# Kernel optimization log

Measured on AMD Instinct MI355X. Metric: run time of the kernel, lower is better.

The kernel has to match this reference:

```python
import jax, jax.numpy as jnp
import numpy as np

B, L, E, H = 4, 1024, 2048, 16
DH = E // H
SCALE_BASE = 512.0


def _rotate_every_two(x):
    x1 = x[..., ::2]
    x2 = x[..., 1::2]
    return jnp.stack([-x2, x1], axis=-1).reshape(x.shape)


def _xpos(x, downscale):
    # x: [BH, L, Dh]; non-incremental path => offset = 0
    length = x.shape[1]
    head_dim = x.shape[-1]
    min_pos = -(length // 2)
    positions = jnp.arange(min_pos, length + min_pos, dtype=jnp.float32)  # [L]
    base = (jnp.arange(0, head_dim, 2, dtype=jnp.float32) + 0.4 * head_dim) / (1.4 * head_dim)  # [Dh/2]
    scale = base[None, :] ** (positions[:, None] / SCALE_BASE)  # [L, Dh/2]
    # fixed_pos_embedding over `scale` (seq_len=L, dim=Dh/2), positions 0..L-1
    dim = head_dim // 2
    inv_freq = 1.0 / (10000.0 ** (jnp.arange(0, dim, dtype=jnp.float32) / dim))
    sinusoid = jnp.arange(length, dtype=jnp.float32)[:, None] * inv_freq[None, :]
    sin, cos = jnp.sin(sinusoid), jnp.cos(sinusoid)
    if downscale:
        scale = 1.0 / scale
    sin_s = jnp.repeat(sin * scale, 2, axis=-1)  # duplicate_interleave -> [L, Dh]
    cos_s = jnp.repeat(cos * scale, 2, axis=-1)
    return x * cos_s + _rotate_every_two(x) * sin_s


def setup_inputs() -> dict:
    key = jax.random.key(0)
    ks = jax.random.split(key, 6)
    w_std = 1.0 / np.sqrt(E)
    query = jax.random.normal(ks[0], (B, L, E), dtype=jnp.float32)
    Wq = jax.random.normal(ks[1], (E, E), dtype=jnp.float32) * w_std
    Wk = jax.random.normal(ks[2], (E, E), dtype=jnp.float32) * w_std
    Wv = jax.random.normal(ks[3], (E, E), dtype=jnp.float32) * w_std
    Wo = jax.random.normal(ks[4], (E, E), dtype=jnp.float32) * w_std
    bq = jnp.zeros((E,), jnp.float32)
    bk = jnp.zeros((E,), jnp.float32)
    bv = jnp.zeros((E,), jnp.float32)
    bo = jnp.zeros((E,), jnp.float32)
    # causal additive mask [L, L]: 0 on/below diag, large negative above
    attn_mask = jnp.where(jnp.triu(jnp.ones((L, L), bool), k=1), -1e9, 0.0).astype(jnp.float32)
    rel_pos = jax.random.normal(ks[5], (B * H, L, L), dtype=jnp.float32) * 0.02
    return {"query": query, "Wq": Wq, "bq": bq, "Wk": Wk, "bk": bk, "Wv": Wv,
            "bv": bv, "Wo": Wo, "bo": bo, "attn_mask": attn_mask, "rel_pos": rel_pos}


def reference(query, Wq, bq, Wk, bk, Wv, bv, Wo, bo, attn_mask, rel_pos):
    scaling = DH ** -0.5
    q = (query @ Wq.T + bq) * scaling
    k = query @ Wk.T + bk
    v = query @ Wv.T + bv

    def split(t):  # [B, L, E] -> [B*H, L, Dh]
        return t.reshape(B, L, H, DH).transpose(0, 2, 1, 3).reshape(B * H, L, DH)

    q, k, v = split(q), split(k), split(v)
    k = _xpos(k, downscale=True)
    q = _xpos(q, downscale=False)

    w = jnp.einsum('btd,bsd->bts', q, k)          # [B*H, L, L]
    w = jnp.nan_to_num(w) + attn_mask[None]
    w = w + rel_pos
    w = jax.nn.softmax(w.astype(jnp.float32), axis=-1).astype(w.dtype)
    attn = jnp.einsum('bts,bsd->btd', w, v)       # [B*H, L, Dh]
    attn = attn.reshape(B, H, L, DH).transpose(0, 2, 1, 3).reshape(B, L, E)
    out = attn @ Wo.T + bo
    attn_weights = w.reshape(B, H, L, L).transpose(1, 0, 2, 3)  # [H, B, L, L]
    return out, attn_weights
```

## Files before the change

### kernel.cpp

```cpp
#include <hip/hip_runtime.h>
#include <math.h>

#define BB 4
#define LL 1024
#define EE 2048
#define HH 16
#define DHD 128
#define NTOK 4096
#define NBH 64
#define OUT0_ELEMS 8388608

typedef __attribute__((ext_vector_type(8))) short short8;
typedef __attribute__((ext_vector_type(4))) float f32x4;
typedef __attribute__((ext_vector_type(4))) unsigned short ushort4v;
typedef __attribute__((ext_vector_type(8))) unsigned short ushort8v;

__device__ __forceinline__ unsigned short f2bf(float x) {
    union { float f; unsigned int u; } v; v.f = x;
    unsigned int r = v.u + 0x7FFFu + ((v.u >> 16) & 1u);
    return (unsigned short)(r >> 16);
}
__device__ __forceinline__ float bf2f(unsigned short h) {
    union { unsigned int u; float f; } v; v.u = ((unsigned int)h) << 16;
    return v.f;
}

__device__ __forceinline__ void gload16(const void* g, void* l) {
    __builtin_amdgcn_global_load_lds((const __attribute__((address_space(1))) void*)g,
                                     (__attribute__((address_space(3))) void*)l,
                                     16, 0, 0);
}

__global__ __launch_bounds__(256) void cvt_k(const float* __restrict__ in,
                                             unsigned short* __restrict__ out, int n) {
    int i = (blockIdx.x * 256 + threadIdx.x) * 8;
    if (i >= n) return;
    float4 a = *(const float4*)(in + i);
    float4 b = *(const float4*)(in + i + 4);
    ushort4v u, w;
    u.x = f2bf(a.x); u.y = f2bf(a.y); u.z = f2bf(a.z); u.w = f2bf(a.w);
    w.x = f2bf(b.x); w.y = f2bf(b.y); w.z = f2bf(b.z); w.w = f2bf(b.w);
    *(ushort4v*)(out + i) = u;
    *(ushort4v*)(out + i + 4) = w;
}

__global__ __launch_bounds__(64) void xpos_table_k(float4* __restrict__ tab) {
    int t = blockIdx.x;
    int j = threadIdx.x;
    float pos = (float)(t - 512);
    float base = (2.0f * (float)j + 51.2f) * (1.0f / 179.2f);
    float sc = powf(base, pos * (1.0f / 512.0f));
    float inv_freq = powf(10000.0f, -(float)j * (1.0f / 64.0f));
    float ang = (float)t * inv_freq;
    float s = sinf(ang);
    float c = cosf(ang);
    tab[(t << 6) | j] = make_float4(c * sc, s * sc, c / sc, s / sc);
}

__global__ __launch_bounds__(256) void xpos_apply_k(unsigned short* __restrict__ q,
                                                    unsigned short* __restrict__ k,
                                                    const float4* __restrict__ tab) {
    int g = blockIdx.x * 256 + threadIdx.x;
    int jj = g & 15;
    int t = (g >> 4) & 1023;
    int bh = g >> 14;
    size_t off = (((size_t)((bh << 10) | t)) << 7) + jj * 8;
    ushort8v qv = *(const ushort8v*)(q + off);
    ushort8v kv = *(const ushort8v*)(k + off);
    ushort8v qo, ko;
#pragma unroll
    for (int p = 0; p < 4; ++p) {
        float4 tb = tab[(t << 6) | (jj * 4 + p)];
        float qx = bf2f(qv[2 * p]), qy = bf2f(qv[2 * p + 1]);
        float kx = bf2f(kv[2 * p]), ky = bf2f(kv[2 * p + 1]);
        qo[2 * p]     = f2bf(qx * tb.x - qy * tb.y);
        qo[2 * p + 1] = f2bf(qy * tb.x + qx * tb.y);
        ko[2 * p]     = f2bf(kx * tb.z - ky * tb.w);
        ko[2 * p + 1] = f2bf(ky * tb.z + kx * tb.w);
    }
    *(ushort8v*)(q + off) = qo;
    *(ushort8v*)(k + off) = ko;
}

template <int MODE>
__global__ __launch_bounds__(256)
void mm_k(const unsigned short* __restrict__ Abf, const unsigned short* __restrict__ Bp,
          const float* __restrict__ bias, void* __restrict__ Cptr, float alpha) {
    __shared__ alignas(16) unsigned short lA[128 * 32];
    __shared__ alignas(16) unsigned short lB[128 * 32];

    const int tid = threadIdx.x;
    const int lane = tid & 63;
    const int wave = tid >> 6;
    const int wr = wave >> 1, wc = wave & 1;
    const int fr = lane & 15, fq = lane >> 4;
    const int m0 = blockIdx.y * 128, n0 = blockIdx.x * 128;

    f32x4 acc[4][4];
#pragma unroll
    for (int i = 0; i < 4; ++i)
#pragma unroll
        for (int j = 0; j < 4; ++j) acc[i][j] = (f32x4){0.f, 0.f, 0.f, 0.f};

    for (int k0 = 0; k0 < 2048; k0 += 32) {
#pragma unroll
        for (int i = 0; i < 2; ++i) {
            int c = i * 256 + tid;
            int r = c >> 2, kc = c & 3;
            gload16(Abf + (size_t)(m0 + r) * 2048 + k0 + kc * 8, &lA[c * 8]);
        }
#pragma unroll
        for (int i = 0; i < 2; ++i) {
            int c = i * 256 + tid;
            int r = c >> 2, kc = c & 3;
            gload16(Bp + (size_t)(n0 + r) * 2048 + k0 + kc * 8, &lB[c * 8]);
        }
        __syncthreads();

        short8 afr[4], bfr[4];
#pragma unroll
        for (int mi = 0; mi < 4; ++mi)
            afr[mi] = *(const short8*)&lA[(wr * 64 + mi * 16 + fr) * 32 + fq * 8];
#pragma unroll
        for (int ni = 0; ni < 4; ++ni)
            bfr[ni] = *(const short8*)&lB[(wc * 64 + ni * 16 + fr) * 32 + fq * 8];
#pragma unroll
        for (int mi = 0; mi < 4; ++mi)
#pragma unroll
            for (int ni = 0; ni < 4; ++ni)
                acc[mi][ni] = __builtin_amdgcn_mfma_f32_16x16x32_bf16(
                    afr[mi], bfr[ni], acc[mi][ni], 0, 0, 0);
        __syncthreads();
    }

#pragma unroll
    for (int mi = 0; mi < 4; ++mi) {
#pragma unroll
        for (int ni = 0; ni < 4; ++ni) {
#pragma unroll
            for (int r = 0; r < 4; ++r) {
                int m = m0 + wr * 64 + mi * 16 + fq * 4 + r;
                int n = n0 + wc * 64 + ni * 16 + fr;
                float v = acc[mi][ni][r];
                if constexpr (MODE == 0 || MODE == 1) {
                    v = alpha * (v + bias[n]);
                    int b_ = m >> 10, t = m & 1023, h = n >> 7, d = n & 127;
                    unsigned short* q = (unsigned short*)Cptr;
                    q[(((size_t)(b_ * HH + h) << 10 | t) << 7) | d] = f2bf(v);
                } else if constexpr (MODE == 2) {
                    v += bias[n];
                    int b_ = m >> 10, t = m & 1023, h = n >> 7, d = n & 127;
                    unsigned short* vt = (unsigned short*)Cptr;
                    vt[((size_t)(b_ * HH + h) * 128 + d) * 1024 + t] = f2bf(v);
                } else {
                    float* C = (float*)Cptr;
                    C[(size_t)m * EE + n] = v + bias[n];
                }
            }
        }
    }
}

__global__ __launch_bounds__(256)
void scores_k(const unsigned short* __restrict__ qb, const unsigned short* __restrict__ kb,
              const float* __restrict__ rel, float* __restrict__ attnP,
              float* __restrict__ psum) {
    __shared__ alignas(16) char smem[16384];
    unsigned short* lA = (unsigned short*)smem;
    unsigned short* lB = (unsigned short*)(smem + 8192);
    float* slab = (float*)smem;

    const int tid = threadIdx.x;
    const int lane = tid & 63, wave = tid >> 6;
    const int wr = wave >> 1, wc = wave & 1;
    const int fr = lane & 15, fq = lane >> 4;

    int idx = blockIdx.x;
    int tt = (int)((sqrtf(8.f * (float)idx + 1.f) - 1.f) * 0.5f);
    while ((tt + 1) * (tt + 2) / 2 <= idx) ++tt;
    while (tt * (tt + 1) / 2 > idx) --tt;
    const int ss = idx - tt * (tt + 1) / 2;
    const int t0 = tt << 7, s0 = ss << 7;
    const int bh = blockIdx.y;
    const int hh = bh & 15, bb = bh >> 4;

    const unsigned short* Q = qb + ((size_t)bh << 17);
    const unsigned short* K = kb + ((size_t)bh << 17);

    f32x4 acc[4][4];
#pragma unroll
    for (int i = 0; i < 4; ++i)
#pragma unroll
        for (int j = 0; j < 4; ++j) acc[i][j] = (f32x4){0.f, 0.f, 0.f, 0.f};

    for (int k0 = 0; k0 < 128; k0 += 32) {
#pragma unroll
        for (int i = 0; i < 2; ++i) {
            int c = i * 256 + tid;
            int r = c >> 2, kc = c & 3;
            gload16(Q + (size_t)(t0 + r) * 128 + k0 + kc * 8, &lA[c * 8]);
        }
#pragma unroll
        for (int i = 0; i < 2; ++i) {
            int c = i * 256 + tid;
            int r = c >> 2, kc = c & 3;
            gload16(K + (size_t)(s0 + r) * 128 + k0 + kc * 8, &lB[c * 8]);
        }
        __syncthreads();

        short8 afr[4], bfr[4];
#pragma unroll
        for (int mi = 0; mi < 4; ++mi)
            afr[mi] = *(const short8*)&lA[(wr * 64 + mi * 16 + fr) * 32 + fq * 8];
#pragma unroll
        for (int ni = 0; ni < 4; ++ni)
            bfr[ni] = *(const short8*)&lB[(wc * 64 + ni * 16 + fr) * 32 + fq * 8];
#pragma unroll
        for (int mi = 0; mi < 4; ++mi)
#pragma unroll
            for (int ni = 0; ni < 4; ++ni)
                acc[mi][ni] = __builtin_amdgcn_mfma_f32_16x16x32_bf16(
                    afr[mi], bfr[ni], acc[mi][ni], 0, 0, 0);
        __syncthreads();
    }

    float* PO = attnP + (((size_t)(hh * BB + bb)) << 20);
    const float* RLb = rel + ((size_t)bh << 20);
#pragma unroll
    for (int sl = 0; sl < 4; ++sl) {
        if (wr == (sl >> 1)) {
#pragma unroll
            for (int mi2 = 0; mi2 < 2; ++mi2) {
                int mi = ((sl & 1) << 1) + mi2;
#pragma unroll
                for (int ni = 0; ni < 4; ++ni)
#pragma unroll
                    for (int r = 0; r < 4; ++r) {
                        int srow = (mi2 << 4) + (fq << 2) + r;
                        int col = (wc << 6) + (ni << 4) + fr;
                        slab[srow * 128 + (col ^ (((srow >> 2) & 3) << 4))] = acc[mi][ni][r];
                    }
            }
        }
        __syncthreads();
        {
            int srow = tid >> 3;
            int tg = t0 + (sl << 5) + srow;
            const float* RL = RLb + ((size_t)tg << 10) + s0;
            float* PR = PO + ((size_t)tg << 10) + s0;
            float rsum = 0.f;
#pragma unroll
            for (int c = 0; c < 4; ++c) {
                int col = ((tid & 7) << 2) + (c << 5);
                float4 sv = *(const float4*)&slab[srow * 128 + (col ^ (((srow >> 2) & 3) << 4))];
                float4 rl = *(const float4*)(RL + col);
                float4 e;
                e.x = (s0 + col     <= tg) ? __expf(sv.x + rl.x - 15.f) : 0.f;
                e.y = (s0 + col + 1 <= tg) ? __expf(sv.y + rl.y - 15.f) : 0.f;
                e.z = (s0 + col + 2 <= tg) ? __expf(sv.z + rl.z - 15.f) : 0.f;
                e.w = (s0 + col + 3 <= tg) ? __expf(sv.w + rl.w - 15.f) : 0.f;
                *(float4*)(PR + col) = e;
                rsum += e.x + e.y + e.z + e.w;
            }
            rsum += __shfl_xor(rsum, 1);
            rsum += __shfl_xor(rsum, 2);
            rsum += __shfl_xor(rsum, 4);
            if ((tid & 7) == 0)
                psum[((((size_t)bh << 10) + tg) << 3) + ss] = rsum;
        }
        __syncthreads();
    }
}

__global__ __launch_bounds__(256)
void pv_k(const float* __restrict__ attnP, const unsigned short* __restrict__ vt,
          const float* __restrict__ psum, unsigned short* __restrict__ am) {
    __shared__ alignas(16) unsigned short lA[128 * 32];
    __shared__ alignas(16) unsigned short lB[128 * 32];
    __shared__ float lInv[128];

    const int tid = threadIdx.x;
    const int lane = tid & 63, wave = tid >> 6;
    const int wr = wave >> 1, wc = wave & 1;
    const int fr = lane & 15, fq = lane >> 4;
    const int tt = 7 - blockIdx.x;
    const int t0 = tt << 7;
    const int bh = blockIdx.y;
    const int hh = bh & 15, bb = bh >> 4;

    const float* PO = attnP + (((size_t)(hh * BB + bb)) << 20) + ((size_t)t0 << 10);
    const unsigned short* Vb = vt + ((size_t)bh << 17);

    if (tid < 128) {
        const float* p = psum + ((((size_t)bh << 10) + t0 + tid) << 3);
        float s = 0.f;
#pragma unroll
        for (int j = 0; j < 8; ++j) s += (j <= tt) ? p[j] : 0.f;
        lInv[tid] = 1.f / s;
    }

    f32x4 acc[4][4];
#pragma unroll
    for (int i = 0; i < 4; ++i)
#pragma unroll
        for (int j = 0; j < 4; ++j) acc[i][j] = (f32x4){0.f, 0.f, 0.f, 0.f};

    const int kend = (tt + 1) << 7;
    for (int k0 = 0; k0 < kend; k0 += 32) {
#pragma unroll
        for (int i = 0; i < 4; ++i) {
            int c = i * 256 + tid;
            int r = c >> 3, cc = c & 7;
            float4 v = *(const float4*)(PO + (size_t)r * 1024 + k0 + cc * 4);
            ushort4v h;
            h.x = f2bf(v.x); h.y = f2bf(v.y); h.z = f2bf(v.z); h.w = f2bf(v.w);
            *(ushort4v*)&lA[r * 32 + cc * 4] = h;
        }
#pragma unroll
        for (int i = 0; i < 2; ++i) {
            int c = i * 256 + tid;
            int r = c >> 2, kc = c & 3;
            gload16(Vb + (size_t)r * 1024 + k0 + kc * 8, &lB[c * 8]);
        }
        __syncthreads();

        short8 afr[4], bfr[4];
#pragma unroll
        for (int mi = 0; mi < 4; ++mi)
            afr[mi] = *(const short8*)&lA[(wr * 64 + mi * 16 + fr) * 32 + fq * 8];
#pragma unroll
        for (int ni = 0; ni < 4; ++ni)
            bfr[ni] = *(const short8*)&lB[(wc * 64 + ni * 16 + fr) * 32 + fq * 8];
#pragma unroll
        for (int mi = 0; mi < 4; ++mi)
#pragma unroll
            for (int ni = 0; ni < 4; ++ni)
                acc[mi][ni] = __builtin_amdgcn_mfma_f32_16x16x32_bf16(
                    afr[mi], bfr[ni], acc[mi][ni], 0, 0, 0);
        __syncthreads();
    }

#pragma unroll
    for (int mi = 0; mi < 4; ++mi)
#pragma unroll
        for (int ni = 0; ni < 4; ++ni)
#pragma unroll
            for (int r = 0; r < 4; ++r) {
                int tl = wr * 64 + mi * 16 + fq * 4 + r;
                int d = wc * 64 + ni * 16 + fr;
                float o = acc[mi][ni][r] * lInv[tl];
                am[(((size_t)(bb * 1024 + t0 + tl)) << 11) + hh * 128 + d] = f2bf(o);
            }
}

__global__ __launch_bounds__(256)
void norm_k(float* __restrict__ attnP, const float* __restrict__ psum) {
    const int tid = threadIdx.x;
    const int lane = tid & 63, wave = tid >> 6;
    const int row = blockIdx.x * 4 + wave;
    const int bh = row >> 10, t = row & 1023;
    const int hh = bh & 15, bb = bh >> 4;
    const int tt = t >> 7;
    float v = (lane < 8 && lane <= tt) ? psum[((size_t)row << 3) + lane] : 0.f;
    v += __shfl_xor(v, 1);
    v += __shfl_xor(v, 2);
    v += __shfl_xor(v, 4);
    float inv = 1.f / __shfl(v, 0);
    float* PR = attnP + (((size_t)(hh * BB + bb)) << 20) + ((size_t)t << 10);
#pragma unroll
    for (int it = 0; it < 4; ++it) {
        int col = it * 256 + lane * 4;
        if (col <= t) {
            float4 x = *(const float4*)(PR + col);
            x.x *= inv; x.y *= inv; x.z *= inv; x.w *= inv;
            *(float4*)(PR + col) = x;
        } else {
            *(float4*)(PR + col) = make_float4(0.f, 0.f, 0.f, 0.f);
        }
    }
}

extern "C" void kernel_launch(void* const* d_in, const int* in_sizes, int n_in,
                              void* d_out, int out_size, void* d_ws, size_t ws_size,
                              hipStream_t stream) {
    const float* query = (const float*)d_in[0];
    const float* Wq    = (const float*)d_in[1];
    const float* bq    = (const float*)d_in[2];
    const float* Wk    = (const float*)d_in[3];
    const float* bk    = (const float*)d_in[4];
    const float* Wv    = (const float*)d_in[5];
    const float* bv    = (const float*)d_in[6];
    const float* Wo    = (const float*)d_in[7];
    const float* bo    = (const float*)d_in[8];
    const float* rel   = (const float*)d_in[10];

    float* out    = (float*)d_out;
    float* attn_w = out + OUT0_ELEMS;

    char* w = (char*)d_ws;
    unsigned short* Xbf = (unsigned short*)(w);
    unsigned short* Wqb = (unsigned short*)(w + (16 << 20));
    unsigned short* Wkb = (unsigned short*)(w + (24 << 20));
    unsigned short* Wvb = (unsigned short*)(w + (32 << 20));
    unsigned short* Wob = (unsigned short*)(w + (40 << 20));
    unsigned short* qb  = (unsigned short*)(w + (48 << 20));
    unsigned short* kb  = (unsigned short*)(w + (64 << 20));
    unsigned short* vt  = (unsigned short*)(w + (80 << 20));
    unsigned short* am  = (unsigned short*)(w + (96 << 20));
    float4* tab         = (float4*)(w + (112 << 20));
    float* psum         = (float*)(w + (113u << 20));

    const float scaling = 0.08838834764831845f;

    xpos_table_k<<<LL, 64, 0, stream>>>(tab);

    cvt_k<<<4096, 256, 0, stream>>>(query, Xbf, OUT0_ELEMS);
    cvt_k<<<2048, 256, 0, stream>>>(Wq, Wqb, EE * EE);
    cvt_k<<<2048, 256, 0, stream>>>(Wk, Wkb, EE * EE);
    cvt_k<<<2048, 256, 0, stream>>>(Wv, Wvb, EE * EE);
    cvt_k<<<2048, 256, 0, stream>>>(Wo, Wob, EE * EE);

    dim3 gproj(EE / 128, NTOK / 128, 1);
    mm_k<0><<<gproj, 256, 0, stream>>>(Xbf, Wqb, bq, qb, scaling);
    mm_k<1><<<gproj, 256, 0, stream>>>(Xbf, Wkb, bk, kb, 1.0f);
    mm_k<2><<<gproj, 256, 0, stream>>>(Xbf, Wvb, bv, vt, 1.0f);

    xpos_apply_k<<<(NBH * LL * 16) / 256, 256, 0, stream>>>(qb, kb, tab);

    dim3 gsc(36, NBH);
    scores_k<<<gsc, 256, 0, stream>>>(qb, kb, rel, attn_w, psum);

    dim3 gpv(8, NBH);
    pv_k<<<gpv, 256, 0, stream>>>(attn_w, vt, psum, am);

    norm_k<<<NBH * LL / 4, 256, 0, stream>>>(attn_w, psum);

    dim3 gout(EE / 128, NTOK / 128, 1);
    mm_k<4><<<gout, 256, 0, stream>>>(am, Wob, bo, out, 1.0f);
}
```

Baseline: 498.8 us.

## Fuse QKV projections into one GEMM and fold softmax normalization into PV

Packs Wq/Wk/Wv contiguously and launches a single QKV projection GEMM over a 3x wider grid, selecting bias, scale and output layout per block. Removes the separate norm kernel by having pv_k scale each probability row by its inverse sum while loading it, write the normalized values back to the attention-weights output, and zero the masked tail region. This avoids one extra full read/write pass over the large fp32 attention tensor and two kernel launches, at the cost of pv_k now doing read-modify-write stores and extra zero-fill stores. Also moves the normalization before the bf16 conversion, changing rounding slightly.

```diff
diff --git a/kernel.cpp b/kernel.cpp
--- a/kernel.cpp
+++ b/kernel.cpp
@@ -82,10 +82,12 @@
     *(ushort8v*)(k + off) = ko;
 }
 
-template <int MODE>
 __global__ __launch_bounds__(256)
-void mm_k(const unsigned short* __restrict__ Abf, const unsigned short* __restrict__ Bp,
-          const float* __restrict__ bias, void* __restrict__ Cptr, float alpha) {
+void mmqkv_k(const unsigned short* __restrict__ Abf, const unsigned short* __restrict__ Wqkv,
+             const float* __restrict__ bq, const float* __restrict__ bk,
+             const float* __restrict__ bv, unsigned short* __restrict__ qb,
+             unsigned short* __restrict__ kb, unsigned short* __restrict__ vt,
+             float scaling) {
     __shared__ alignas(16) unsigned short lA[128 * 32];
     __shared__ alignas(16) unsigned short lB[128 * 32];
 
@@ -95,6 +97,9 @@
     const int wr = wave >> 1, wc = wave & 1;
     const int fr = lane & 15, fq = lane >> 4;
     const int m0 = blockIdx.y * 128, n0 = blockIdx.x * 128;
+    const int w = n0 >> 11;
+    const float* bsel = (w == 0) ? bq : (w == 1) ? bk : bv;
+    const float alpha = (w == 0) ? scaling : 1.0f;
 
     f32x4 acc[4][4];
 #pragma unroll
@@ -113,7 +118,7 @@
         for (int i = 0; i < 2; ++i) {
             int c = i * 256 + tid;
             int r = c >> 2, kc = c & 3;
-            gload16(Bp + (size_t)(n0 + r) * 2048 + k0 + kc * 8, &lB[c * 8]);
+            gload16(Wqkv + (size_t)(n0 + r) * 2048 + k0 + kc * 8, &lB[c * 8]);
         }
         __syncthreads();
 
@@ -141,24 +146,80 @@
             for (int r = 0; r < 4; ++r) {
                 int m = m0 + wr * 64 + mi * 16 + fq * 4 + r;
                 int n = n0 + wc * 64 + ni * 16 + fr;
-                float v = acc[mi][ni][r];
-                if constexpr (MODE == 0 || MODE == 1) {
-                    v = alpha * (v + bias[n]);
-                    int b_ = m >> 10, t = m & 1023, h = n >> 7, d = n & 127;
-                    unsigned short* q = (unsigned short*)Cptr;
-                    q[(((size_t)(b_ * HH + h) << 10 | t) << 7) | d] = f2bf(v);
-                } else if constexpr (MODE == 2) {
-                    v += bias[n];
-                    int b_ = m >> 10, t = m & 1023, h = n >> 7, d = n & 127;
-                    unsigned short* vt = (unsigned short*)Cptr;
-                    vt[((size_t)(b_ * HH + h) * 128 + d) * 1024 + t] = f2bf(v);
-                } else {
-                    float* C = (float*)Cptr;
-                    C[(size_t)m * EE + n] = v + bias[n];
-                }
+                int nn = n & 2047;
+                int b_ = m >> 10, t = m & 1023, h = nn >> 7, d = nn & 127;
+                float v = alpha * (acc[mi][ni][r] + bsel[nn]);
+                if (w == 0)
+                    qb[(((size_t)(b_ * HH + h) << 10 | t) << 7) | d] = f2bf(v);
+                else if (w == 1)
+                    kb[(((size_t)(b_ * HH + h) << 10 | t) << 7) | d] = f2bf(v);
+                else
+                    vt[((size_t)((b_ * HH + h) * 128 + d) << 10) | t] = f2bf(v);
             }
         }
     }
+}
+
+__global__ __launch_bounds__(256)
+void mmo_k(const unsigned short* __restrict__ Abf, const unsigned short* __restrict__ Bp,
+           const float* __restrict__ bias, float* __restrict__ C) {
+    __shared__ alignas(16) unsigned short lA[128 * 32];
+    __shared__ alignas(16) unsigned short lB[128 * 32];
+
+    const int tid = threadIdx.x;
+    const int lane = tid & 63;
+    const int wave = tid >> 6;
+    const int wr = wave >> 1, wc = wave & 1;
+    const int fr = lane & 15, fq = lane >> 4;
+    const int m0 = blockIdx.y * 128, n0 = blockIdx.x * 128;
+
+    f32x4 acc[4][4];
+#pragma unroll
+    for (int i = 0; i < 4; ++i)
+#pragma unroll
+        for (int j = 0; j < 4; ++j) acc[i][j] = (f32x4){0.f, 0.f, 0.f, 0.f};
+
+    for (int k0 = 0; k0 < 2048; k0 += 32) {
+#pragma unroll
+        for (int i = 0; i < 2; ++i) {
+            int c = i * 256 + tid;
+            int r = c >> 2, kc = c & 3;
+            gload16(Abf + (size_t)(m0 + r) * 2048 + k0 + kc * 8, &lA[c * 8]);
+        }
+#pragma unroll
+        for (int i = 0; i < 2; ++i) {
+            int c = i * 256 + tid;
+            int r = c >> 2, kc = c & 3;
+            gload16(Bp + (size_t)(n0 + r) * 2048 + k0 + kc * 8, &lB[c * 8]);
+        }
+        __syncthreads();
+
+        short8 afr[4], bfr[4];
+#pragma unroll
+        for (int mi = 0; mi < 4; ++mi)
+            afr[mi] = *(const short8*)&lA[(wr * 64 + mi * 16 + fr) * 32 + fq * 8];
+#pragma unroll
+        for (int ni = 0; ni < 4; ++ni)
+            bfr[ni] = *(const short8*)&lB[(wc * 64 + ni * 16 + fr) * 32 + fq * 8];
+#pragma unroll
+        for (int mi = 0; mi < 4; ++mi)
+#pragma unroll
+            for (int ni = 0; ni < 4; ++ni)
+                acc[mi][ni] = __builtin_amdgcn_mfma_f32_16x16x32_bf16(
+                    afr[mi], bfr[ni], acc[mi][ni], 0, 0, 0);
+        __syncthreads();
+    }
+
+#pragma unroll
+    for (int mi = 0; mi < 4; ++mi)
+#pragma unroll
+        for (int ni = 0; ni < 4; ++ni)
+#pragma unroll
+            for (int r = 0; r < 4; ++r) {
+                int m = m0 + wr * 64 + mi * 16 + fq * 4 + r;
+                int n = n0 + wc * 64 + ni * 16 + fr;
+                C[(size_t)m * EE + n] = acc[mi][ni][r] + bias[n];
+            }
 }
 
 __global__ __launch_bounds__(256)
@@ -273,7 +334,7 @@
 }
 
 __global__ __launch_bounds__(256)
-void pv_k(const float* __restrict__ attnP, const unsigned short* __restrict__ vt,
+void pv_k(float* __restrict__ attnP, const unsigned short* __restrict__ vt,
           const float* __restrict__ psum, unsigned short* __restrict__ am) {
     __shared__ alignas(16) unsigned short lA[128 * 32];
     __shared__ alignas(16) unsigned short lB[128 * 32];
@@ -288,7 +349,7 @@
     const int bh = blockIdx.y;
     const int hh = bh & 15, bb = bh >> 4;
 
-    const float* PO = attnP + (((size_t)(hh * BB + bb)) << 20) + ((size_t)t0 << 10);
+    float* PO = attnP + (((size_t)(hh * BB + bb)) << 20) + ((size_t)t0 << 10);
     const unsigned short* Vb = vt + ((size_t)bh << 17);
 
     if (tid < 128) {
@@ -298,6 +359,7 @@
         for (int j = 0; j < 8; ++j) s += (j <= tt) ? p[j] : 0.f;
         lInv[tid] = 1.f / s;
     }
+    __syncthreads();
 
     f32x4 acc[4][4];
 #pragma unroll
@@ -311,7 +373,11 @@
         for (int i = 0; i < 4; ++i) {
             int c = i * 256 + tid;
             int r = c >> 3, cc = c & 7;
-            float4 v = *(const float4*)(PO + (size_t)r * 1024 + k0 + cc * 4);
+            float* gp = PO + (size_t)r * 1024 + k0 + cc * 4;
+            float4 v = *(const float4*)gp;
+            float inv = lInv[r];
+            v.x *= inv; v.y *= inv; v.z *= inv; v.w *= inv;
+            *(float4*)gp = v;
             ushort4v h;
             h.x = f2bf(v.x); h.y = f2bf(v.y); h.z = f2bf(v.z); h.w = f2bf(v.w);
             *(ushort4v*)&lA[r * 32 + cc * 4] = h;
@@ -348,35 +414,15 @@
             for (int r = 0; r < 4; ++r) {
                 int tl = wr * 64 + mi * 16 + fq * 4 + r;
                 int d = wc * 64 + ni * 16 + fr;
-                float o = acc[mi][ni][r] * lInv[tl];
-                am[(((size_t)(bb * 1024 + t0 + tl)) << 11) + hh * 128 + d] = f2bf(o);
+                am[(((size_t)(bb * 1024 + t0 + tl)) << 11) + hh * 128 + d] =
+                    f2bf(acc[mi][ni][r]);
             }
-}
-
-__global__ __launch_bounds__(256)
-void norm_k(float* __restrict__ attnP, const float* __restrict__ psum) {
-    const int tid = threadIdx.x;
-    const int lane = tid & 63, wave = tid >> 6;
-    const int row = blockIdx.x * 4 + wave;
-    const int bh = row >> 10, t = row & 1023;
-    const int hh = bh & 15, bb = bh >> 4;
-    const int tt = t >> 7;
-    float v = (lane < 8 && lane <= tt) ? psum[((size_t)row << 3) + lane] : 0.f;
-    v += __shfl_xor(v, 1);
-    v += __shfl_xor(v, 2);
-    v += __shfl_xor(v, 4);
-    float inv = 1.f / __shfl(v, 0);
-    float* PR = attnP + (((size_t)(hh * BB + bb)) << 20) + ((size_t)t << 10);
-#pragma unroll
-    for (int it = 0; it < 4; ++it) {
-        int col = it * 256 + lane * 4;
-        if (col <= t) {
-            float4 x = *(const float4*)(PR + col);
-            x.x *= inv; x.y *= inv; x.z *= inv; x.w *= inv;
-            *(float4*)(PR + col) = x;
-        } else {
-            *(float4*)(PR + col) = make_float4(0.f, 0.f, 0.f, 0.f);
-        }
+
+    if (kend < 1024) {
+        float4 z = make_float4(0.f, 0.f, 0.f, 0.f);
+        for (int rr = wave; rr < 128; rr += 4)
+            for (int c = kend + lane * 4; c < 1024; c += 256)
+                *(float4*)(PO + (size_t)rr * 1024 + c) = z;
     }
 }
 
@@ -398,32 +444,28 @@
     float* attn_w = out + OUT0_ELEMS;
 
     char* w = (char*)d_ws;
-    unsigned short* Xbf = (unsigned short*)(w);
-    unsigned short* Wqb = (unsigned short*)(w + (16 << 20));
-    unsigned short* Wkb = (unsigned short*)(w + (24 << 20));
-    unsigned short* Wvb = (unsigned short*)(w + (32 << 20));
-    unsigned short* Wob = (unsigned short*)(w + (40 << 20));
-    unsigned short* qb  = (unsigned short*)(w + (48 << 20));
-    unsigned short* kb  = (unsigned short*)(w + (64 << 20));
-    unsigned short* vt  = (unsigned short*)(w + (80 << 20));
-    unsigned short* am  = (unsigned short*)(w + (96 << 20));
-    float4* tab         = (float4*)(w + (112 << 20));
-    float* psum         = (float*)(w + (113u << 20));
+    unsigned short* Xbf   = (unsigned short*)(w);
+    unsigned short* Wqkvb = (unsigned short*)(w + (16 << 20));
+    unsigned short* Wob   = (unsigned short*)(w + (40 << 20));
+    unsigned short* qb    = (unsigned short*)(w + (48 << 20));
+    unsigned short* kb    = (unsigned short*)(w + (64 << 20));
+    unsigned short* vt    = (unsigned short*)(w + (80 << 20));
+    unsigned short* am    = (unsigned short*)(w + (96 << 20));
+    float4* tab           = (float4*)(w + (112 << 20));
+    float* psum           = (float*)(w + (113u << 20));
 
     const float scaling = 0.08838834764831845f;
 
     xpos_table_k<<<LL, 64, 0, stream>>>(tab);
 
     cvt_k<<<4096, 256, 0, stream>>>(query, Xbf, OUT0_ELEMS);
-    cvt_k<<<2048, 256, 0, stream>>>(Wq, Wqb, EE * EE);
-    cvt_k<<<2048, 256, 0, stream>>>(Wk, Wkb, EE * EE);
-    cvt_k<<<2048, 256, 0, stream>>>(Wv, Wvb, EE * EE);
+    cvt_k<<<2048, 256, 0, stream>>>(Wq, Wqkvb, EE * EE);
+    cvt_k<<<2048, 256, 0, stream>>>(Wk, Wqkvb + (size_t)EE * EE, EE * EE);
+    cvt_k<<<2048, 256, 0, stream>>>(Wv, Wqkvb + 2 * (size_t)EE * EE, EE * EE);
     cvt_k<<<2048, 256, 0, stream>>>(Wo, Wob, EE * EE);
 
-    dim3 gproj(EE / 128, NTOK / 128, 1);
-    mm_k<0><<<gproj, 256, 0, stream>>>(Xbf, Wqb, bq, qb, scaling);
-    mm_k<1><<<gproj, 256, 0, stream>>>(Xbf, Wkb, bk, kb, 1.0f);
-    mm_k<2><<<gproj, 256, 0, stream>>>(Xbf, Wvb, bv, vt, 1.0f);
+    dim3 gqkv(3 * EE / 128, NTOK / 128);
+    mmqkv_k<<<gqkv, 256, 0, stream>>>(Xbf, Wqkvb, bq, bk, bv, qb, kb, vt, scaling);
 
     xpos_apply_k<<<(NBH * LL * 16) / 256, 256, 0, stream>>>(qb, kb, tab);
 
@@ -433,8 +475,6 @@
     dim3 gpv(8, NBH);
     pv_k<<<gpv, 256, 0, stream>>>(attn_w, vt, psum, am);
 
-    norm_k<<<NBH * LL / 4, 256, 0, stream>>>(attn_w, psum);
-
-    dim3 gout(EE / 128, NTOK / 128, 1);
-    mm_k<4><<<gout, 256, 0, stream>>>(am, Wob, bo, out, 1.0f);
-}
+    dim3 gout(EE / 128, NTOK / 128);
+    mmo_k<<<gout, 256, 0, stream>>>(am, Wob, bo, out);
+}
```

New measurement: 536.2 us. 1.07x slower.
